# Performance work log

Hardware: AMD Instinct MI355X
Metric: run time of the kernel (lower is better)

Reference implementation:

```python
import jax, jax.numpy as jnp
import numpy as np

NUM_HEADS = 16
MASKED_BIAS = -10000.0


def setup_inputs() -> dict:
    key = jax.random.key(0)
    ks = jax.random.split(key, 5)
    B, S, D = 4, 2048, 1024
    return {
        "encodings": jax.random.normal(ks[0], (B, S, D), dtype=jnp.float32),
        "w_attn": jax.random.normal(ks[1], (D, 3 * D), dtype=jnp.float32) * (1.0 / np.sqrt(D)),
        "b_attn": jax.random.normal(ks[2], (3 * D,), dtype=jnp.float32) * 0.02,
        "w_proj": jax.random.normal(ks[3], (D, D), dtype=jnp.float32) * (1.0 / np.sqrt(D)),
        "b_proj": jax.random.normal(ks[4], (D,), dtype=jnp.float32) * 0.02,
    }


def reference(encodings, w_attn, b_attn, w_proj, b_proj):
    B, S, D = encodings.shape
    H = NUM_HEADS
    hs = D // H
    qkv = encodings @ w_attn + b_attn            # [B,S,3D]
    q, k, v = jnp.split(qkv, 3, axis=-1)
    # 'b s (h c) -> b h s c'
    def split_heads(x):
        return x.reshape(B, S, H, hs).transpose(0, 2, 1, 3)
    q, k, v = split_heads(q), split_heads(k), split_heads(v)
    # scores[b,h,f,t] = q[t] . k[f] / sqrt(hs)  (f=key, t=query)
    scores = jnp.einsum('bhtc,bhfc->bhft', q, k) / np.sqrt(hs).astype(jnp.float32)
    # causal: query t may attend key f iff t >= f  -> upper-tri in (f,t)
    causal = jnp.triu(jnp.ones((S, S), dtype=bool))  # [f,t]
    scores = jnp.where(causal[None, None], scores, jnp.asarray(MASKED_BIAS, scores.dtype))
    attn = jax.nn.softmax(scores, axis=-2)       # softmax over keys (f)
    ctx = jnp.einsum('bhft,bhfc->bhtc', attn, v)  # [B,H,S,hs]
    ctx = ctx.transpose(0, 2, 1, 3).reshape(B, S, D)  # 'b h s c -> b s (h c)'
    return ctx @ w_proj + b_proj
```

## Files before the change

### kernel.cpp

```cpp
#include <hip/hip_runtime.h>
#include <hip/hip_bf16.h>
#include <stdint.h>

#define NH  16
#define SEQ 2048
#define DM  1024
#define HS  64
#define NB  4

typedef __attribute__((ext_vector_type(8))) short bf16x8;
typedef __attribute__((ext_vector_type(4))) float f32x4;

__device__ __forceinline__ unsigned short f2b(float f) {
    unsigned int u = __float_as_uint(f);
    u += 0x7fffu + ((u >> 16) & 1u);
    return (unsigned short)(u >> 16);
}

__device__ __forceinline__ void gload16(const void* g, void* lds) {
    __builtin_amdgcn_global_load_lds(
        (const __attribute__((address_space(1))) unsigned int*)g,
        (__attribute__((address_space(3))) unsigned int*)lds,
        16, 0, 0);
}

__global__ void k_cvt(const float* __restrict__ in, unsigned short* __restrict__ out, int n) {
    int i = (blockIdx.x * blockDim.x + threadIdx.x) * 4;
    if (i >= n) return;
    float4 v = *(const float4*)(in + i);
    ushort4 o;
    o.x = f2b(v.x); o.y = f2b(v.y); o.z = f2b(v.z); o.w = f2b(v.w);
    *(ushort4*)(out + i) = o;
}

__global__ void k_tr(const float* __restrict__ in, unsigned short* __restrict__ out, int K, int N) {
    __shared__ float t[32][33];
    int n0 = blockIdx.x * 32, k0 = blockIdx.y * 32;
    int tx = threadIdx.x, ty = threadIdx.y;
#pragma unroll
    for (int j = 0; j < 32; j += 8)
        t[ty + j][tx] = in[(size_t)(k0 + ty + j) * N + n0 + tx];
    __syncthreads();
#pragma unroll
    for (int j = 0; j < 32; j += 8)
        out[(size_t)(n0 + ty + j) * K + k0 + tx] = f2b(t[tx][ty + j]);
}

template <int MODE>
__global__ __launch_bounds__(256, 2) void k_gemm(
    const unsigned short* __restrict__ A,
    const unsigned short* __restrict__ Bt,
    const float* __restrict__ bias,
    void* __restrict__ outp, int M, int N, int K)
{
    __shared__ unsigned short As[128 * 64];
    __shared__ unsigned short Bs[128 * 64];
    const int tid = threadIdx.x;
    const int l = tid & 63, w = tid >> 6;
    const int lg = l >> 4, li = l & 15;
    const int m0 = blockIdx.x * 128, n0 = blockIdx.y * 128;
    const int wm = (w >> 1) * 64, wn = (w & 1) * 64;

    f32x4 acc[4][4] = {};

    for (int k0 = 0; k0 < K; k0 += 64) {
#pragma unroll
        for (int i = 0; i < 4; i++) {
            int ch = i * 256 + tid;
            int row = ch >> 3, cc = ch & 7;
            int sc = cc ^ (row & 7);
            gload16(A + (size_t)(m0 + row) * K + k0 + sc * 8, &As[(i * 256 + w * 64) * 8]);
        }
#pragma unroll
        for (int i = 0; i < 4; i++) {
            int ch = i * 256 + tid;
            int row = ch >> 3, cc = ch & 7;
            int sc = cc ^ (row & 7);
            gload16(Bt + (size_t)(n0 + row) * K + k0 + sc * 8, &Bs[(i * 256 + w * 64) * 8]);
        }
        __syncthreads();
#pragma unroll
        for (int kc = 0; kc < 2; kc++) {
            bf16x8 af[4], bfr[4];
#pragma unroll
            for (int mi = 0; mi < 4; mi++) {
                int row = wm + mi * 16 + li;
                int chunk = (kc * 4 + lg) ^ (row & 7);
                af[mi] = *(const bf16x8*)&As[row * 64 + chunk * 8];
            }
#pragma unroll
            for (int ni = 0; ni < 4; ni++) {
                int row = wn + ni * 16 + li;
                int chunk = (kc * 4 + lg) ^ (row & 7);
                bfr[ni] = *(const bf16x8*)&Bs[row * 64 + chunk * 8];
            }
#pragma unroll
            for (int mi = 0; mi < 4; mi++)
#pragma unroll
                for (int ni = 0; ni < 4; ni++)
                    acc[mi][ni] = __builtin_amdgcn_mfma_f32_16x16x32_bf16(af[mi], bfr[ni], acc[mi][ni], 0, 0, 0);
        }
        __syncthreads();
    }

#pragma unroll
    for (int mi = 0; mi < 4; mi++) {
        int mrow = m0 + wm + mi * 16 + lg * 4;
#pragma unroll
        for (int ni = 0; ni < 4; ni++) {
            int col = n0 + wn + ni * 16 + li;
            float bv = bias[col];
            if (MODE == 0) {
                float* out = (float*)outp;
#pragma unroll
                for (int r = 0; r < 4; r++)
                    out[(size_t)(mrow + r) * N + col] = acc[mi][ni][r] + bv;
            } else {
                unsigned short* out = (unsigned short*)outp;
                const size_t QKV1 = (size_t)NB * NH * SEQ * HS;
                int sqkv = col >> 10;
                int d = col & 1023;
                int h = d >> 6, c = d & 63;
                float scale = (sqkv == 0) ? 0.125f : 1.0f;
#pragma unroll
                for (int r = 0; r < 4; r++) {
                    int m = mrow + r;
                    int bq = m >> 11, sp = m & 2047;
                    size_t off;
                    if (sqkv == 2)
                        off = 2 * QKV1 + ((size_t)(bq * NH + h) * HS + c) * SEQ + sp;
                    else
                        off = (size_t)sqkv * QKV1 + ((size_t)(bq * NH + h) * SEQ + sp) * HS + c;
                    out[off] = f2b((acc[mi][ni][r] + bv) * scale);
                }
            }
        }
    }
}

__global__ __launch_bounds__(256) void k_attn(
    const unsigned short* __restrict__ qkv,
    unsigned short* __restrict__ ctx)
{
    __shared__ unsigned short Ks[64 * 64];
    __shared__ unsigned short Vts[64 * 64];
    __shared__ unsigned short Ps[4 * 32 * 64];
    const int tid = threadIdx.x;
    const int l = tid & 63, w = tid >> 6;
    const int lg = l >> 4, li = l & 15;
    const int bh = blockIdx.x;
    const int q0 = (gridDim.y - 1 - blockIdx.y) * 128;
    const size_t hb = (size_t)bh * SEQ * HS;
    const size_t QKV1 = (size_t)NB * NH * SEQ * HS;
    const unsigned short* Qg = qkv + hb;
    const unsigned short* Kg = qkv + QKV1 + hb;
    const unsigned short* VTg = qkv + 2 * QKV1 + hb;

    bf16x8 aq[2][2];
#pragma unroll
    for (int rt = 0; rt < 2; rt++) {
        int t = q0 + rt * 64 + w * 16 + li;
        aq[rt][0] = *(const bf16x8*)(Qg + (size_t)t * HS + lg * 8);
        aq[rt][1] = *(const bf16x8*)(Qg + (size_t)t * HS + 32 + lg * 8);
    }

    f32x4 acc[2][4] = {};
    float mr[2][4], ls[2][4];
#pragma unroll
    for (int rt = 0; rt < 2; rt++)
#pragma unroll
        for (int r = 0; r < 4; r++) { mr[rt][r] = -1e30f; ls[rt][r] = 0.f; }

    const int ntiles = q0 / 64 + 2;

    for (int ft = 0; ft < ntiles; ft++) {
        int f0 = ft * 64;
#pragma unroll
        for (int i = 0; i < 2; i++) {
            int ch = i * 256 + tid;
            int row = ch >> 3, cc = ch & 7;
            int sc = cc ^ (row & 7);
            gload16(Kg + (size_t)(f0 + row) * HS + sc * 8, &Ks[(i * 256 + w * 64) * 8]);
        }
#pragma unroll
        for (int i = 0; i < 2; i++) {
            int ch = i * 256 + tid;
            int row = ch >> 3, cc = ch & 7;
            int sc = cc ^ (row & 7);
            gload16(VTg + (size_t)row * SEQ + f0 + sc * 8, &Vts[(i * 256 + w * 64) * 8]);
        }
        __syncthreads();

#pragma unroll
        for (int rt = 0; rt < 2; rt++) {
            const int tb = q0 + rt * 64 + w * 16;
            if (f0 > tb + 15) continue;

            f32x4 sa[4] = {};
#pragma unroll
            for (int kc = 0; kc < 2; kc++)
#pragma unroll
                for (int nt = 0; nt < 4; nt++) {
                    int row = nt * 16 + li;
                    int chunk = (kc * 4 + lg) ^ (row & 7);
                    bf16x8 bk = *(const bf16x8*)&Ks[row * 64 + chunk * 8];
                    sa[nt] = __builtin_amdgcn_mfma_f32_16x16x32_bf16(aq[rt][kc], bk, sa[nt], 0, 0, 0);
                }

            if (f0 + 63 > tb) {
                int trow = tb + lg * 4;
#pragma unroll
                for (int nt = 0; nt < 4; nt++) {
                    int f = f0 + nt * 16 + li;
#pragma unroll
                    for (int r = 0; r < 4; r++)
                        if (f > trow + r) sa[nt][r] = -1e30f;
                }
            }

            float corr[4];
#pragma unroll
            for (int r = 0; r < 4; r++) {
                float rm = fmaxf(fmaxf(sa[0][r], sa[1][r]), fmaxf(sa[2][r], sa[3][r]));
                rm = fmaxf(rm, __shfl_xor(rm, 1));
                rm = fmaxf(rm, __shfl_xor(rm, 2));
                rm = fmaxf(rm, __shfl_xor(rm, 4));
                rm = fmaxf(rm, __shfl_xor(rm, 8));
                float mn = fmaxf(mr[rt][r], rm);
                corr[r] = __expf(mr[rt][r] - mn);
                mr[rt][r] = mn;
            }
            float rs[4] = {0.f, 0.f, 0.f, 0.f};
#pragma unroll
            for (int nt = 0; nt < 4; nt++)
#pragma unroll
                for (int r = 0; r < 4; r++) {
                    float p = __expf(sa[nt][r] - mr[rt][r]);
                    sa[nt][r] = p;
                    rs[r] += p;
                }
#pragma unroll
            for (int r = 0; r < 4; r++) {
                rs[r] += __shfl_xor(rs[r], 1);
                rs[r] += __shfl_xor(rs[r], 2);
                rs[r] += __shfl_xor(rs[r], 4);
                rs[r] += __shfl_xor(rs[r], 8);
                ls[rt][r] = ls[rt][r] * corr[r] + rs[r];
            }
#pragma unroll
            for (int nt = 0; nt < 4; nt++)
#pragma unroll
                for (int r = 0; r < 4; r++)
                    acc[rt][nt][r] *= corr[r];

            char* PB = (char*)Ps + w * 4096 + rt * 2048;
#pragma unroll
            for (int nt = 0; nt < 4; nt++)
#pragma unroll
                for (int r = 0; r < 4; r++) {
                    int row = lg * 4 + r, f = nt * 16 + li;
                    *(unsigned short*)(PB + row * 128 + ((f * 2) ^ ((row & 7) << 4))) = f2b(sa[nt][r]);
                }

#pragma unroll
            for (int kc = 0; kc < 2; kc++) {
                int C = kc * 4 + lg;
                bf16x8 pf = *(const bf16x8*)(PB + li * 128 + ((C * 16) ^ ((li & 7) << 4)));
#pragma unroll
                for (int nt = 0; nt < 4; nt++) {
                    int c = nt * 16 + li;
                    int vch = C ^ (c & 7);
                    bf16x8 vf = *(const bf16x8*)&Vts[c * 64 + vch * 8];
                    acc[rt][nt] = __builtin_amdgcn_mfma_f32_16x16x32_bf16(pf, vf, acc[rt][nt], 0, 0, 0);
                }
            }
        }
        __syncthreads();
    }

    int b = bh >> 4, h = bh & 15;
#pragma unroll
    for (int rt = 0; rt < 2; rt++)
#pragma unroll
        for (int nt = 0; nt < 4; nt++)
#pragma unroll
            for (int r = 0; r < 4; r++) {
                int t = q0 + rt * 64 + w * 16 + lg * 4 + r;
                int c = nt * 16 + li;
                float v = acc[rt][nt][r] / ls[rt][r];
                ctx[((size_t)(b * SEQ + t)) * DM + h * HS + c] = f2b(v);
            }
}

extern "C" void kernel_launch(void* const* d_in, const int* in_sizes, int n_in,
                              void* d_out, int out_size, void* d_ws, size_t ws_size,
                              hipStream_t stream) {
    const float* enc    = (const float*)d_in[0];
    const float* w_attn = (const float*)d_in[1];
    const float* b_attn = (const float*)d_in[2];
    const float* w_proj = (const float*)d_in[3];
    const float* b_proj = (const float*)d_in[4];
    float* out = (float*)d_out;

    unsigned short* ws = (unsigned short*)d_ws;
    unsigned short* X    = ws;
    unsigned short* Wq   = ws + 8388608;
    unsigned short* Wp   = Wq + 3145728;
    unsigned short* QKV  = Wp + 1048576;
    unsigned short* CTX  = X;

    const int M = NB * SEQ;

    k_cvt<<<8192, 256, 0, stream>>>(enc, X, M * DM);
    k_tr<<<dim3(96, 32), dim3(32, 8), 0, stream>>>(w_attn, Wq, DM, 3 * DM);
    k_tr<<<dim3(32, 32), dim3(32, 8), 0, stream>>>(w_proj, Wp, DM, DM);
    k_gemm<1><<<dim3(M / 128, 24), 256, 0, stream>>>(X, Wq, b_attn, QKV, M, 3 * DM, DM);
    k_attn<<<dim3(NB * NH, SEQ / 64 / 2), 256, 0, stream>>>(QKV, CTX);
    k_gemm<0><<<dim3(M / 128, 8), 256, 0, stream>>>(CTX, Wp, b_proj, out, M, DM, DM);
}
```

Baseline: 322.3 us.

## Pair causal query blocks per workgroup, double-buffer K/V, use lazy exp2 rescaling

Each attention workgroup now handles two query blocks, a short one and its mirror long one, so causal work is balanced and each K/V tile load serves both. K/V tiles are double-buffered in LDS so the next tile's global->LDS copy overlaps compute. Softmax switches to exp2 with log2e folded into the Q scale. It also skips rescaling unless the running max grows by more than 8, and truncates P to bf16 instead of rounding. This cuts exp and rescale ALU work, at the cost of more registers, a smaller grid, and slightly less precise P values.

```diff
diff --git a/kernel.cpp b/kernel.cpp
--- a/kernel.cpp
+++ b/kernel.cpp
@@ -121,7 +121,7 @@
                 int sqkv = col >> 10;
                 int d = col & 1023;
                 int h = d >> 6, c = d & 63;
-                float scale = (sqkv == 0) ? 0.125f : 1.0f;
+                float scale = (sqkv == 0) ? 0.18033688f : 1.0f;
 #pragma unroll
                 for (int r = 0; r < 4; r++) {
                     int m = mrow + r;
@@ -138,59 +138,67 @@
     }
 }
 
-__global__ __launch_bounds__(256) void k_attn(
+__global__ __launch_bounds__(256, 2) void k_attn(
     const unsigned short* __restrict__ qkv,
     unsigned short* __restrict__ ctx)
 {
-    __shared__ unsigned short Ks[64 * 64];
-    __shared__ unsigned short Vts[64 * 64];
+    __shared__ unsigned short Ks[2][64 * 64];
+    __shared__ unsigned short Vts[2][64 * 64];
     __shared__ unsigned short Ps[4 * 32 * 64];
     const int tid = threadIdx.x;
     const int l = tid & 63, w = tid >> 6;
     const int lg = l >> 4, li = l & 15;
     const int bh = blockIdx.x;
-    const int q0 = (gridDim.y - 1 - blockIdx.y) * 128;
+    const int qa = blockIdx.y;
+    const int qb = 15 - qa;
+    const int qA0 = qa * 128, qB0 = qb * 128;
+    const int na = qA0 / 64 + 2, nbt = qB0 / 64 + 2;
     const size_t hb = (size_t)bh * SEQ * HS;
     const size_t QKV1 = (size_t)NB * NH * SEQ * HS;
     const unsigned short* Qg = qkv + hb;
     const unsigned short* Kg = qkv + QKV1 + hb;
     const unsigned short* VTg = qkv + 2 * QKV1 + hb;
 
-    bf16x8 aq[2][2];
+    bf16x8 aqA[2][2], aqB[2][2];
 #pragma unroll
     for (int rt = 0; rt < 2; rt++) {
-        int t = q0 + rt * 64 + w * 16 + li;
-        aq[rt][0] = *(const bf16x8*)(Qg + (size_t)t * HS + lg * 8);
-        aq[rt][1] = *(const bf16x8*)(Qg + (size_t)t * HS + 32 + lg * 8);
+        int tA = qA0 + rt * 64 + w * 16 + li;
+        aqA[rt][0] = *(const bf16x8*)(Qg + (size_t)tA * HS + lg * 8);
+        aqA[rt][1] = *(const bf16x8*)(Qg + (size_t)tA * HS + 32 + lg * 8);
+        int tB = qB0 + rt * 64 + w * 16 + li;
+        aqB[rt][0] = *(const bf16x8*)(Qg + (size_t)tB * HS + lg * 8);
+        aqB[rt][1] = *(const bf16x8*)(Qg + (size_t)tB * HS + 32 + lg * 8);
     }
 
-    f32x4 acc[2][4] = {};
-    float mr[2][4], ls[2][4];
+    f32x4 accA[2][4] = {}, accB[2][4] = {};
+    float mrA[2][4], lsA[2][4], mrB[2][4], lsB[2][4];
 #pragma unroll
     for (int rt = 0; rt < 2; rt++)
 #pragma unroll
-        for (int r = 0; r < 4; r++) { mr[rt][r] = -1e30f; ls[rt][r] = 0.f; }
-
-    const int ntiles = q0 / 64 + 2;
-
-    for (int ft = 0; ft < ntiles; ft++) {
-        int f0 = ft * 64;
+        for (int r = 0; r < 4; r++) {
+            mrA[rt][r] = -1e30f; lsA[rt][r] = 0.f;
+            mrB[rt][r] = -1e30f; lsB[rt][r] = 0.f;
+        }
+
+    auto stage = [&](int buf, int f0) {
 #pragma unroll
         for (int i = 0; i < 2; i++) {
             int ch = i * 256 + tid;
             int row = ch >> 3, cc = ch & 7;
             int sc = cc ^ (row & 7);
-            gload16(Kg + (size_t)(f0 + row) * HS + sc * 8, &Ks[(i * 256 + w * 64) * 8]);
+            gload16(Kg + (size_t)(f0 + row) * HS + sc * 8, &Ks[buf][(i * 256 + w * 64) * 8]);
         }
 #pragma unroll
         for (int i = 0; i < 2; i++) {
             int ch = i * 256 + tid;
             int row = ch >> 3, cc = ch & 7;
             int sc = cc ^ (row & 7);
-            gload16(VTg + (size_t)row * SEQ + f0 + sc * 8, &Vts[(i * 256 + w * 64) * 8]);
-        }
-        __syncthreads();
-
+            gload16(VTg + (size_t)row * SEQ + f0 + sc * 8, &Vts[buf][(i * 256 + w * 64) * 8]);
+        }
+    };
+
+    auto process = [&](int q0, bf16x8 (&aq)[2][2], f32x4 (&acc)[2][4],
+                       float (&mr)[2][4], float (&ls)[2][4], int f0, int buf) {
 #pragma unroll
         for (int rt = 0; rt < 2; rt++) {
             const int tb = q0 + rt * 64 + w * 16;
@@ -203,7 +211,7 @@
                 for (int nt = 0; nt < 4; nt++) {
                     int row = nt * 16 + li;
                     int chunk = (kc * 4 + lg) ^ (row & 7);
-                    bf16x8 bk = *(const bf16x8*)&Ks[row * 64 + chunk * 8];
+                    bf16x8 bk = *(const bf16x8*)&Ks[buf][row * 64 + chunk * 8];
                     sa[nt] = __builtin_amdgcn_mfma_f32_16x16x32_bf16(aq[rt][kc], bk, sa[nt], 0, 0, 0);
                 }
 
@@ -218,7 +226,7 @@
                 }
             }
 
-            float corr[4];
+            float pmax[4];
 #pragma unroll
             for (int r = 0; r < 4; r++) {
                 float rm = fmaxf(fmaxf(sa[0][r], sa[1][r]), fmaxf(sa[2][r], sa[3][r]));
@@ -226,16 +234,33 @@
                 rm = fmaxf(rm, __shfl_xor(rm, 2));
                 rm = fmaxf(rm, __shfl_xor(rm, 4));
                 rm = fmaxf(rm, __shfl_xor(rm, 8));
-                float mn = fmaxf(mr[rt][r], rm);
-                corr[r] = __expf(mr[rt][r] - mn);
-                mr[rt][r] = mn;
-            }
+                pmax[r] = rm;
+            }
+            bool need = false;
+#pragma unroll
+            for (int r = 0; r < 4; r++) need |= (pmax[r] > mr[rt][r] + 8.0f);
+            if (__any(need)) {
+                float corr[4];
+#pragma unroll
+                for (int r = 0; r < 4; r++) {
+                    float mn = fmaxf(mr[rt][r], pmax[r]);
+                    corr[r] = __builtin_amdgcn_exp2f(mr[rt][r] - mn);
+                    mr[rt][r] = mn;
+                    ls[rt][r] *= corr[r];
+                }
+#pragma unroll
+                for (int nt = 0; nt < 4; nt++)
+#pragma unroll
+                    for (int r = 0; r < 4; r++)
+                        acc[rt][nt][r] *= corr[r];
+            }
+
             float rs[4] = {0.f, 0.f, 0.f, 0.f};
 #pragma unroll
             for (int nt = 0; nt < 4; nt++)
 #pragma unroll
                 for (int r = 0; r < 4; r++) {
-                    float p = __expf(sa[nt][r] - mr[rt][r]);
+                    float p = __builtin_amdgcn_exp2f(sa[nt][r] - mr[rt][r]);
                     sa[nt][r] = p;
                     rs[r] += p;
                 }
@@ -245,13 +270,8 @@
                 rs[r] += __shfl_xor(rs[r], 2);
                 rs[r] += __shfl_xor(rs[r], 4);
                 rs[r] += __shfl_xor(rs[r], 8);
-                ls[rt][r] = ls[rt][r] * corr[r] + rs[r];
-            }
-#pragma unroll
-            for (int nt = 0; nt < 4; nt++)
-#pragma unroll
-                for (int r = 0; r < 4; r++)
-                    acc[rt][nt][r] *= corr[r];
+                ls[rt][r] += rs[r];
+            }
 
             char* PB = (char*)Ps + w * 4096 + rt * 2048;
 #pragma unroll
@@ -259,7 +279,8 @@
 #pragma unroll
                 for (int r = 0; r < 4; r++) {
                     int row = lg * 4 + r, f = nt * 16 + li;
-                    *(unsigned short*)(PB + row * 128 + ((f * 2) ^ ((row & 7) << 4))) = f2b(sa[nt][r]);
+                    *(unsigned short*)(PB + row * 128 + ((f * 2) ^ ((row & 7) << 4))) =
+                        (unsigned short)(__float_as_uint(sa[nt][r]) >> 16);
                 }
 
 #pragma unroll
@@ -270,11 +291,20 @@
                 for (int nt = 0; nt < 4; nt++) {
                     int c = nt * 16 + li;
                     int vch = C ^ (c & 7);
-                    bf16x8 vf = *(const bf16x8*)&Vts[c * 64 + vch * 8];
+                    bf16x8 vf = *(const bf16x8*)&Vts[buf][c * 64 + vch * 8];
                     acc[rt][nt] = __builtin_amdgcn_mfma_f32_16x16x32_bf16(pf, vf, acc[rt][nt], 0, 0, 0);
                 }
             }
         }
+    };
+
+    stage(0, 0);
+    __syncthreads();
+    for (int ft = 0; ft < nbt; ft++) {
+        int buf = ft & 1;
+        if (ft + 1 < nbt) stage(buf ^ 1, (ft + 1) * 64);
+        process(qB0, aqB, accB, mrB, lsB, ft * 64, buf);
+        if (ft < na) process(qA0, aqA, accA, mrA, lsA, ft * 64, buf);
         __syncthreads();
     }
 
@@ -285,10 +315,11 @@
         for (int nt = 0; nt < 4; nt++)
 #pragma unroll
             for (int r = 0; r < 4; r++) {
-                int t = q0 + rt * 64 + w * 16 + lg * 4 + r;
                 int c = nt * 16 + li;
-                float v = acc[rt][nt][r] / ls[rt][r];
-                ctx[((size_t)(b * SEQ + t)) * DM + h * HS + c] = f2b(v);
+                int tB = qB0 + rt * 64 + w * 16 + lg * 4 + r;
+                ctx[((size_t)(b * SEQ + tB)) * DM + h * HS + c] = f2b(accB[rt][nt][r] / lsB[rt][r]);
+                int tA = qA0 + rt * 64 + w * 16 + lg * 4 + r;
+                ctx[((size_t)(b * SEQ + tA)) * DM + h * HS + c] = f2b(accA[rt][nt][r] / lsA[rt][r]);
             }
 }
 
@@ -315,6 +346,6 @@
     k_tr<<<dim3(96, 32), dim3(32, 8), 0, stream>>>(w_attn, Wq, DM, 3 * DM);
     k_tr<<<dim3(32, 32), dim3(32, 8), 0, stream>>>(w_proj, Wp, DM, DM);
     k_gemm<1><<<dim3(M / 128, 24), 256, 0, stream>>>(X, Wq, b_attn, QKV, M, 3 * DM, DM);
-    k_attn<<<dim3(NB * NH, SEQ / 64 / 2), 256, 0, stream>>>(QKV, CTX);
+    k_attn<<<dim3(NB * NH, 8), 256, 0, stream>>>(QKV, CTX);
     k_gemm<0><<<dim3(M / 128, 8), 256, 0, stream>>>(CTX, Wp, b_proj, out, M, DM, DM);
 }
```

Result: faster. 307.2 us (-4.7%).
